# Performance work log

Measured on AMD Instinct MI355X. Metric: run time of the kernel, lower is better.

## Reference

```python
import jax, jax.numpy as jnp
import numpy as np

EPS = 1e-12  # torch F.normalize default eps


def _l2norm(x):
    n = jnp.linalg.norm(x, axis=-1, keepdims=True)
    return x / jnp.maximum(n, EPS)


def setup_inputs() -> dict:
    key = jax.random.key(0)
    k1, k2 = jax.random.split(key)
    B, D = 8192, 1024
    img_emb = jax.random.normal(k1, (B, D), dtype=jnp.float32)
    txt_emb = jax.random.normal(k2, (B, D), dtype=jnp.float32)
    t_prime = jnp.asarray(np.log(1.0 / 0.1), dtype=jnp.float32)  # log(1/temperature_init)
    bias = jnp.asarray(-10.0, dtype=jnp.float32)
    return {"img_emb": img_emb, "txt_emb": txt_emb, "t_prime": t_prime, "bias": bias}


def reference(img_emb, txt_emb, t_prime, bias):
    img = _l2norm(img_emb)
    txt = _l2norm(txt_emb)
    t = jnp.minimum(jnp.exp(t_prime), 100.0)
    logits = jnp.einsum('id,jd->ij', img, txt) * t + bias  # [B, B]
    B = img.shape[0]
    # STANDARD mode: labels = 2*I - 1
    labels = 2.0 * jnp.eye(B, dtype=logits.dtype) - 1.0
    loss = -jnp.sum(jax.nn.log_sigmoid(labels * logits)) / B
    return loss
```

## Files before the change

kernel.cpp:

```cpp
#include <hip/hip_runtime.h>
#include <hip/hip_bf16.h>

#define B_SZ 8192
#define D_SZ 1024

typedef __attribute__((ext_vector_type(4))) float floatx4;
typedef __attribute__((ext_vector_type(8))) int   int8v;
typedef __attribute__((ext_vector_type(4))) int   int4v;

__device__ __forceinline__ void glds16(const void* g, void* l) {
    __builtin_amdgcn_global_load_lds(
        (const __attribute__((address_space(1))) void*)g,
        (__attribute__((address_space(3))) void*)l, 16, 0, 0);
}

__global__ __launch_bounds__(256) void norm_cast_fp8(
    const float* __restrict__ img, const float* __restrict__ txt,
    unsigned char* __restrict__ imgQ, unsigned char* __restrict__ txtQ,
    float* __restrict__ out)
{
    if (blockIdx.x == 0 && threadIdx.x == 0) *out = 0.0f;

    const int lane = threadIdx.x & 63;
    int w = blockIdx.x * 4 + (threadIdx.x >> 6);
    const float* src; unsigned char* dst;
    if (w < B_SZ) { src = img + (size_t)w * D_SZ; dst = imgQ + (size_t)w * D_SZ; }
    else { w -= B_SZ; src = txt + (size_t)w * D_SZ; dst = txtQ + (size_t)w * D_SZ; }

    float4 v[4];
    float ss = 0.0f;
    #pragma unroll
    for (int i = 0; i < 4; ++i) {
        v[i] = ((const float4*)src)[lane + 64 * i];
        ss += v[i].x*v[i].x + v[i].y*v[i].y + v[i].z*v[i].z + v[i].w*v[i].w;
    }
    #pragma unroll
    for (int off = 1; off < 64; off <<= 1) ss += __shfl_xor(ss, off, 64);
    const float scale = 1.0f / fmaxf(sqrtf(ss), 1e-12f);

    #pragma unroll
    for (int i = 0; i < 4; ++i) {
        int packed = 0;
        packed = __builtin_amdgcn_cvt_pk_fp8_f32(v[i].x * scale, v[i].y * scale, packed, false);
        packed = __builtin_amdgcn_cvt_pk_fp8_f32(v[i].z * scale, v[i].w * scale, packed, true);
        ((int*)dst)[lane + 64 * i] = packed;
    }
}

__global__ __launch_bounds__(256, 2) void siglip_gemm_loss_fp8(
    const unsigned char* __restrict__ A,
    const unsigned char* __restrict__ Bt,
    const float* __restrict__ tp, const float* __restrict__ bp,
    float* __restrict__ out)
{
    __shared__ __align__(16) unsigned char As[2][2][256 * 64];
    __shared__ __align__(16) unsigned char Bs[2][128 * 64];

    const int tid  = threadIdx.x;
    const int lane = tid & 63;
    const int wave = tid >> 6;
    const int wm = wave & 1, wn = wave >> 1;
    const int bi = blockIdx.x * 256;
    const int bj = blockIdx.y * 128;
    const int quad = lane >> 4;
    const int l16  = lane & 15;

    floatx4 acc[8][4];
    #pragma unroll
    for (int i = 0; i < 8; ++i)
        #pragma unroll
        for (int j = 0; j < 4; ++j)
            acc[i][j] = (floatx4){0.f, 0.f, 0.f, 0.f};

    auto stage_a = [&](int k0, int buf) {
        #pragma unroll
        for (int it = 0; it < 4; ++it) {
            int s = tid + it * 256;
            int row = s >> 2, p = s & 3;
            int g = p ^ ((row >> 1) & 3);
            const unsigned char* ga = A + ((size_t)(bi + row) * D_SZ + k0 + g * 16);
            glds16(ga,      As[buf][0] + s * 16);
            glds16(ga + 64, As[buf][1] + s * 16);
        }
    };
    auto stage_b = [&](int k0) {
        #pragma unroll
        for (int it = 0; it < 2; ++it) {
            int s = tid + it * 256;
            int row = s >> 2, p = s & 3;
            int g = p ^ ((row >> 1) & 3);
            const unsigned char* gb = Bt + ((size_t)(bj + row) * D_SZ + k0 + g * 16);
            glds16(gb,      Bs[0] + s * 16);
            glds16(gb + 64, Bs[1] + s * 16);
        }
    };

    const int sw   = (l16 >> 1) & 3;
    const int hsel = quad >> 1;
    const int p0   = ((quad & 1) * 2) ^ sw;
    const int p1   = p0 ^ 1;

    stage_a(0, 0);
    stage_b(0);

    for (int kk = 0; kk < D_SZ / 128; ++kk) {
        __syncthreads();
        const int buf = kk & 1;

        int8v bfr[4];
        #pragma unroll
        for (int nt = 0; nt < 4; ++nt) {
            int r = wn * 64 + nt * 16 + l16;
            int4v lo = *(const int4v*)(Bs[hsel] + r * 64 + p0 * 16);
            int4v hi = *(const int4v*)(Bs[hsel] + r * 64 + p1 * 16);
            bfr[nt][0]=lo[0]; bfr[nt][1]=lo[1]; bfr[nt][2]=lo[2]; bfr[nt][3]=lo[3];
            bfr[nt][4]=hi[0]; bfr[nt][5]=hi[1]; bfr[nt][6]=hi[2]; bfr[nt][7]=hi[3];
        }
        __syncthreads();

        if (kk + 1 < D_SZ / 128) {
            stage_a((kk + 1) * 128, buf ^ 1);
            stage_b((kk + 1) * 128);
        }

        #pragma unroll
        for (int mt = 0; mt < 8; ++mt) {
            int r = wm * 128 + mt * 16 + l16;
            int4v lo = *(const int4v*)(As[buf][hsel] + r * 64 + p0 * 16);
            int4v hi = *(const int4v*)(As[buf][hsel] + r * 64 + p1 * 16);
            int8v af;
            af[0]=lo[0]; af[1]=lo[1]; af[2]=lo[2]; af[3]=lo[3];
            af[4]=hi[0]; af[5]=hi[1]; af[6]=hi[2]; af[7]=hi[3];
            #pragma unroll
            for (int nt = 0; nt < 4; ++nt)
                acc[mt][nt] = __builtin_amdgcn_mfma_scale_f32_16x16x128_f8f6f4(
                    af, bfr[nt], acc[mt][nt],
                    0, 0,
                    0, 127,
                    0, 127);
        }
    }

    const float t    = fminf(__expf(tp[0]), 100.0f);
    const float bias = bp[0];
    float lsum = 0.0f;
    #pragma unroll
    for (int mt = 0; mt < 8; ++mt) {
        #pragma unroll
        for (int nt = 0; nt < 4; ++nt) {
            const int jj = bj + wn * 64 + nt * 16 + l16;
            #pragma unroll
            for (int r = 0; r < 4; ++r) {
                const int ii = bi + wm * 128 + mt * 16 + quad * 4 + r;
                float logit = fmaf(acc[mt][nt][r], t, bias);
                float z = (ii == jj) ? logit : -logit;
                float e = __expf(-fabsf(z));
                lsum += fmaxf(-z, 0.0f) + __logf(1.0f + e);
            }
        }
    }
    #pragma unroll
    for (int off = 32; off > 0; off >>= 1) lsum += __shfl_down(lsum, off, 64);

    __shared__ float red[4];
    if (lane == 0) red[wave] = lsum;
    __syncthreads();
    if (tid == 0)
        atomicAdd(out, (red[0] + red[1] + red[2] + red[3]) * (1.0f / (float)B_SZ));
}

extern "C" void kernel_launch(void* const* d_in, const int* in_sizes, int n_in,
                              void* d_out, int out_size, void* d_ws, size_t ws_size,
                              hipStream_t stream) {
    const float* img = (const float*)d_in[0];
    const float* txt = (const float*)d_in[1];
    const float* tp  = (const float*)d_in[2];
    const float* bp  = (const float*)d_in[3];
    float* out = (float*)d_out;

    unsigned char* imgQ = (unsigned char*)d_ws;
    unsigned char* txtQ = imgQ + (size_t)B_SZ * D_SZ;

    norm_cast_fp8<<<(2 * B_SZ) / 4, 256, 0, stream>>>(img, txt, imgQ, txtQ, out);
    dim3 grid(B_SZ / 256, B_SZ / 128);
    siglip_gemm_loss_fp8<<<grid, 256, 0, stream>>>(imgQ, txtQ, tp, bp, out);
}
```

Before: 229.7 us.

## Enlarge GEMM block tile to 256x256 with 8 waves and double-buffered B

Each workgroup now computes a 256x256 output tile with 512 threads (8 waves) instead of 256x128 with 4 waves, roughly halving redundant global and LDS staging of the FP8 operands. The B operand is now double-buffered like A, so the next k-slice prefetch is issued right after a single barrier per iteration instead of after a second barrier. The cost is 128KB of LDS per block, limiting it to one block per CU. The launch bound of (512, 2) asks for a tighter per-wave register budget while each wave still holds 128 accumulator floats, which risks register spills.

```diff
diff --git a/kernel.cpp b/kernel.cpp
--- a/kernel.cpp
+++ b/kernel.cpp
@@ -47,21 +47,22 @@
     }
 }
 
-__global__ __launch_bounds__(256, 2) void siglip_gemm_loss_fp8(
+__global__ __launch_bounds__(512, 2) void siglip_gemm_loss_fp8(
     const unsigned char* __restrict__ A,
     const unsigned char* __restrict__ Bt,
     const float* __restrict__ tp, const float* __restrict__ bp,
     float* __restrict__ out)
 {
     __shared__ __align__(16) unsigned char As[2][2][256 * 64];
-    __shared__ __align__(16) unsigned char Bs[2][128 * 64];
+    __shared__ __align__(16) unsigned char Bs[2][2][256 * 64];
 
     const int tid  = threadIdx.x;
     const int lane = tid & 63;
     const int wave = tid >> 6;
-    const int wm = wave & 1, wn = wave >> 1;
+    const int wm = wave & 1;
+    const int wn = wave >> 1;
     const int bi = blockIdx.x * 256;
-    const int bj = blockIdx.y * 128;
+    const int bj = blockIdx.y * 256;
     const int quad = lane >> 4;
     const int l16  = lane & 15;
 
@@ -72,26 +73,18 @@
         for (int j = 0; j < 4; ++j)
             acc[i][j] = (floatx4){0.f, 0.f, 0.f, 0.f};
 
-    auto stage_a = [&](int k0, int buf) {
+    auto stage = [&](int k0, int buf) {
         #pragma unroll
-        for (int it = 0; it < 4; ++it) {
-            int s = tid + it * 256;
+        for (int it = 0; it < 2; ++it) {
+            int s = tid + it * 512;
             int row = s >> 2, p = s & 3;
             int g = p ^ ((row >> 1) & 3);
-            const unsigned char* ga = A + ((size_t)(bi + row) * D_SZ + k0 + g * 16);
+            const unsigned char* ga = A  + ((size_t)(bi + row) * D_SZ + k0 + g * 16);
+            const unsigned char* gb = Bt + ((size_t)(bj + row) * D_SZ + k0 + g * 16);
             glds16(ga,      As[buf][0] + s * 16);
             glds16(ga + 64, As[buf][1] + s * 16);
-        }
-    };
-    auto stage_b = [&](int k0) {
-        #pragma unroll
-        for (int it = 0; it < 2; ++it) {
-            int s = tid + it * 256;
-            int row = s >> 2, p = s & 3;
-            int g = p ^ ((row >> 1) & 3);
-            const unsigned char* gb = Bt + ((size_t)(bj + row) * D_SZ + k0 + g * 16);
-            glds16(gb,      Bs[0] + s * 16);
-            glds16(gb + 64, Bs[1] + s * 16);
+            glds16(gb,      Bs[buf][0] + s * 16);
+            glds16(gb + 64, Bs[buf][1] + s * 16);
         }
     };
 
@@ -100,27 +93,23 @@
     const int p0   = ((quad & 1) * 2) ^ sw;
     const int p1   = p0 ^ 1;
 
-    stage_a(0, 0);
-    stage_b(0);
+    stage(0, 0);
 
     for (int kk = 0; kk < D_SZ / 128; ++kk) {
+        const int buf = kk & 1;
         __syncthreads();
-        const int buf = kk & 1;
+
+        if (kk + 1 < D_SZ / 128)
+            stage((kk + 1) * 128, buf ^ 1);
 
         int8v bfr[4];
         #pragma unroll
         for (int nt = 0; nt < 4; ++nt) {
             int r = wn * 64 + nt * 16 + l16;
-            int4v lo = *(const int4v*)(Bs[hsel] + r * 64 + p0 * 16);
-            int4v hi = *(const int4v*)(Bs[hsel] + r * 64 + p1 * 16);
+            int4v lo = *(const int4v*)(Bs[buf][hsel] + r * 64 + p0 * 16);
+            int4v hi = *(const int4v*)(Bs[buf][hsel] + r * 64 + p1 * 16);
             bfr[nt][0]=lo[0]; bfr[nt][1]=lo[1]; bfr[nt][2]=lo[2]; bfr[nt][3]=lo[3];
             bfr[nt][4]=hi[0]; bfr[nt][5]=hi[1]; bfr[nt][6]=hi[2]; bfr[nt][7]=hi[3];
-        }
-        __syncthreads();
-
-        if (kk + 1 < D_SZ / 128) {
-            stage_a((kk + 1) * 128, buf ^ 1);
-            stage_b((kk + 1) * 128);
         }
 
         #pragma unroll
@@ -162,11 +151,15 @@
     #pragma unroll
     for (int off = 32; off > 0; off >>= 1) lsum += __shfl_down(lsum, off, 64);
 
-    __shared__ float red[4];
+    __shared__ float red[8];
     if (lane == 0) red[wave] = lsum;
     __syncthreads();
-    if (tid == 0)
-        atomicAdd(out, (red[0] + red[1] + red[2] + red[3]) * (1.0f / (float)B_SZ));
+    if (tid == 0) {
+        float s = 0.0f;
+        #pragma unroll
+        for (int i = 0; i < 8; ++i) s += red[i];
+        atomicAdd(out, s * (1.0f / (float)B_SZ));
+    }
 }
 
 extern "C" void kernel_launch(void* const* d_in, const int* in_sizes, int n_in,
@@ -182,6 +175,6 @@
     unsigned char* txtQ = imgQ + (size_t)B_SZ * D_SZ;
 
     norm_cast_fp8<<<(2 * B_SZ) / 4, 256, 0, stream>>>(img, txt, imgQ, txtQ, out);
-    dim3 grid(B_SZ / 256, B_SZ / 128);
-    siglip_gemm_loss_fp8<<<grid, 256, 0, stream>>>(imgQ, txtQ, tp, bp, out);
+    dim3 grid(B_SZ / 256, B_SZ / 256);
+    siglip_gemm_loss_fp8<<<grid, 512, 0, stream>>>(imgQ, txtQ, tp, bp, out);
 }
```

After: 192.5 us. 1.19x faster.
